# Optimization experiments

Measured on AMD Instinct MI355X. Metric: run time of the kernel, lower is better.

## Reference

```python
import jax, jax.numpy as jnp
import numpy as np

B, T, C, HS = 4, 512, 128, 64

def setup_inputs() -> dict:
    key = jax.random.key(0)
    ks = jax.random.split(key, 8)
    s1 = 1.0 / np.sqrt(2 * C)  # torch Linear default init scale ~ U(-1/sqrt(in),1/sqrt(in))
    s2 = 1.0 / np.sqrt(C)
    return {
        "x": jax.random.normal(ks[0], (B, T, C), jnp.float32),
        "pos_emb": jax.random.normal(ks[1], (T, C), jnp.float32),
        # att2 layer 1: Linear(2C -> C); stored as [2C, C] (in, out)
        "W1": jax.random.uniform(ks[2], (2 * C, C), jnp.float32, -s1, s1),
        "b1": jax.random.uniform(ks[3], (C,), jnp.float32, -s1, s1),
        # att2 layer 2: Linear(C -> 1)
        "W2": jax.random.uniform(ks[4], (C, 1), jnp.float32, -s2, s2),
        "b2": jax.random.uniform(ks[5], (1,), jnp.float32, -s2, s2),
        # value: Linear(C -> HS, bias=False)
        "Wv": jax.random.uniform(ks[6], (C, HS), jnp.float32, -s2, s2),
    }


def reference(x, pos_emb, W1, b1, W2, b2, Wv):
    b, t, c = x.shape
    x1 = pos_emb + x  # [b,t,c]
    # Pairwise feature: cat([x1[j], x1[i]], -1) at position [i, j].
    # First Linear on the concat splits into two [c,c] blocks -> avoids
    # materializing the [b,t,t,2c] concat while computing identical math.
    W1k, W1q = W1[:c], W1[c:]            # rows for k-part (x1[j]) and q-part (x1[i])
    Ak = jnp.einsum('bjc,cd->bjd', x1, W1k)  # [b,t,c] contribution from key index j
    Aq = jnp.einsum('bic,cd->bid', x1, W1q)  # [b,t,c] contribution from query index i
    hidden = jax.nn.relu(Aq[:, :, None, :] + Ak[:, None, :, :] + b1)  # [b,t,t,c]
    wei = (jnp.einsum('bijc,co->bijo', hidden, W2)[..., 0] + b2[0]) * (c ** -0.5)  # [b,t,t]
    # causal mask (tril)
    mask = jnp.tril(jnp.ones((t, t), dtype=bool))
    wei = jnp.where(mask, wei, -jnp.inf)
    wei = jax.nn.softmax(wei, axis=-1)
    v = jnp.einsum('btc,ch->bth', x, Wv)  # [b,t,hs]
    out = jnp.einsum('bij,bjh->bih', wei, v)
    return out
```

## Files before the change

kernel.cpp:

```cpp
#include <hip/hip_runtime.h>
#include <math.h>

#define B_ 4
#define T_ 512
#define C_ 128
#define HS_ 64

typedef float f4 __attribute__((ext_vector_type(4)));

#define SCALE_ 0.08838834764831845f

__global__ __launch_bounds__(640) void k_prep(
    const float* __restrict__ x, const float* __restrict__ pos,
    const float* __restrict__ W1, const float* __restrict__ b1,
    const float* __restrict__ Wv,
    float* __restrict__ Aq, float* __restrict__ AkT, float* __restrict__ V)
{
    __shared__ float x1s[8 * 132];
    __shared__ float xs[8 * 132];
    const int t = threadIdx.x;
    const int row0 = blockIdx.x * 8;

    if (t < 256) {
        int r = t >> 5, cq = t & 31;
        int gr = row0 + r;
        f4 xv = *(const f4*)(x + gr * 128 + cq * 4);
        f4 pv = *(const f4*)(pos + (gr & 511) * 128 + cq * 4);
        *(f4*)&xs[r * 132 + cq * 4] = xv;
        *(f4*)&x1s[r * 132 + cq * 4] = xv + pv;
    }
    __syncthreads();

    const int q = t >> 3;
    const int r = t & 7;

    const float* wbase;
    int wstr, col0;
    const float* xb;
    f4 binit = {0.f, 0.f, 0.f, 0.f};
    if (q < 32) {
        col0 = q * 4;
        wbase = W1 + 128 * 128 + col0;
        wstr = 128;
        xb = x1s;
        binit = *(const f4*)(b1 + col0);
    } else if (q < 64) {
        col0 = (q - 32) * 4;
        wbase = W1 + col0;
        wstr = 128;
        xb = x1s;
    } else {
        col0 = (q - 64) * 4;
        wbase = Wv + col0;
        wstr = 64;
        xb = xs;
    }

    f4 acc = binit;
    const float* xr = xb + r * 132;
#pragma unroll 8
    for (int c = 0; c < 128; ++c) {
        f4 w = *(const f4*)(wbase + c * wstr);
        acc += xr[c] * w;
    }

    const int gr = row0 + r;
    if (q < 32) {
        *(f4*)(Aq + (size_t)gr * 128 + col0) = acc;
    } else if (q < 64) {
        const int bb = gr >> 9, j = gr & 511;
        float* base = AkT + ((size_t)bb * 128 + col0) * 512 + j;
        base[0]    = acc.x;
        base[512]  = acc.y;
        base[1024] = acc.z;
        base[1536] = acc.w;
    } else {
        *(f4*)(V + (size_t)gr * 64 + col0) = acc;
    }
}

__global__ __launch_bounds__(256) void k_fusedp(
    const float* __restrict__ Aq, const float* __restrict__ AkT,
    const float* __restrict__ V, const float* __restrict__ W2,
    float* __restrict__ pml, float* __restrict__ pacc)
{
    __shared__ float aks[128][64];
    __shared__ float aqs[16][128];
    __shared__ float w2s[128];
    __shared__ float pbuf[4][4][64];

    const int t = threadIdx.x;
    const int b = blockIdx.y;
    const int f = blockIdx.x;

    int n = (int)((1.0f + sqrtf(1.0f + 2.0f * (float)f)) * 0.5f);
    while (2 * n * (n - 1) > f) --n;
    while (2 * n * (n + 1) <= f) ++n;
    const int rem = f - 2 * n * (n - 1);
    const int G = 4 * (n - 1) + rem / n;
    const int w = rem % n;
    const int j0 = w * 64;
    const int row0 = G * 16;

    const float* aktw = AkT + (size_t)b * 128 * 512 + j0;
    for (int idx = t; idx < 2048; idx += 256) {
        int c = idx >> 4, qq = idx & 15;
        *(f4*)&aks[c][qq * 4] = *(const f4*)(aktw + (size_t)c * 512 + qq * 4);
    }
    const float* aqg = Aq + (size_t)(b * 512 + row0) * 128;
    for (int idx = t; idx < 512; idx += 256) {
        int r = idx >> 5, cq = idx & 31;
        *(f4*)&aqs[r][cq * 4] = *(const f4*)(aqg + r * 128 + cq * 4);
    }
    if (t < 32) *(f4*)&w2s[t * 4] = *(const f4*)(W2 + t * 4);
    __syncthreads();

    const int w8 = t >> 6;
    const int lane = t & 63;
    const int rb = 4 * w8;
    const int r0 = row0 + rb, r1 = r0 + 1, r2 = r0 + 2, r3 = r0 + 3;
    const int gj = j0 + lane;

    float m0 = -1e30f, m1 = -1e30f, m2 = -1e30f, m3 = -1e30f;
    float l0 = 0.f, l1 = 0.f, l2 = 0.f, l3 = 0.f;
    float a0 = 0.f, a1 = 0.f, a2 = 0.f, a3 = 0.f;

    if (r3 >= j0) {
        float s0 = 0.f, s1 = 0.f, s2 = 0.f, s3 = 0.f;
#pragma unroll 4
        for (int c = 0; c < 128; ++c) {
            const float ak = aks[c][lane];
            const float wv = w2s[c];
            s0 += fmaxf(ak + aqs[rb + 0][c], 0.f) * wv;
            s1 += fmaxf(ak + aqs[rb + 1][c], 0.f) * wv;
            s2 += fmaxf(ak + aqs[rb + 2][c], 0.f) * wv;
            s3 += fmaxf(ak + aqs[rb + 3][c], 0.f) * wv;
        }
        s0 = (gj <= r0) ? s0 * SCALE_ : -1e30f;
        s1 = (gj <= r1) ? s1 * SCALE_ : -1e30f;
        s2 = (gj <= r2) ? s2 * SCALE_ : -1e30f;
        s3 = (gj <= r3) ? s3 * SCALE_ : -1e30f;

        float t0 = s0, t1 = s1, t2 = s2, t3 = s3;
#pragma unroll
        for (int off = 1; off < 64; off <<= 1) {
            t0 = fmaxf(t0, __shfl_xor(t0, off));
            t1 = fmaxf(t1, __shfl_xor(t1, off));
            t2 = fmaxf(t2, __shfl_xor(t2, off));
            t3 = fmaxf(t3, __shfl_xor(t3, off));
        }
        const float p0 = __expf(s0 - t0);
        const float p1 = __expf(s1 - t1);
        const float p2 = __expf(s2 - t2);
        const float p3 = __expf(s3 - t3);
        pbuf[w8][0][lane] = p0;
        pbuf[w8][1][lane] = p1;
        pbuf[w8][2][lane] = p2;
        pbuf[w8][3][lane] = p3;
        float u0 = p0, u1 = p1, u2 = p2, u3 = p3;
#pragma unroll
        for (int off = 1; off < 64; off <<= 1) {
            u0 += __shfl_xor(u0, off);
            u1 += __shfl_xor(u1, off);
            u2 += __shfl_xor(u2, off);
            u3 += __shfl_xor(u3, off);
        }

        const float* vt = V + ((size_t)b * 512 + j0) * 64 + lane;
        float b0 = 0.f, b1v = 0.f, b2v = 0.f, b3 = 0.f;
#pragma unroll 4
        for (int q4 = 0; q4 < 16; ++q4) {
            f4 q0 = *(const f4*)&pbuf[w8][0][q4 * 4];
            f4 q1 = *(const f4*)&pbuf[w8][1][q4 * 4];
            f4 q2 = *(const f4*)&pbuf[w8][2][q4 * 4];
            f4 q3 = *(const f4*)&pbuf[w8][3][q4 * 4];
            const float v0 = vt[(q4 * 4 + 0) * 64];
            const float v1 = vt[(q4 * 4 + 1) * 64];
            const float v2 = vt[(q4 * 4 + 2) * 64];
            const float v3 = vt[(q4 * 4 + 3) * 64];
            b0  += q0.x * v0 + q0.y * v1 + q0.z * v2 + q0.w * v3;
            b1v += q1.x * v0 + q1.y * v1 + q1.z * v2 + q1.w * v3;
            b2v += q2.x * v0 + q2.y * v1 + q2.z * v2 + q2.w * v3;
            b3  += q3.x * v0 + q3.y * v1 + q3.z * v2 + q3.w * v3;
        }

        const bool c0 = (r0 >= j0), c1 = (r1 >= j0), c2 = (r2 >= j0);
        m0 = c0 ? t0 : -1e30f;  l0 = c0 ? u0 : 0.f;  a0 = c0 ? b0 : 0.f;
        m1 = c1 ? t1 : -1e30f;  l1 = c1 ? u1 : 0.f;  a1 = c1 ? b1v : 0.f;
        m2 = c2 ? t2 : -1e30f;  l2 = c2 ? u2 : 0.f;  a2 = c2 ? b2v : 0.f;
        m3 = t3;                l3 = u3;             a3 = b3;
    }

    const size_t k0 = ((size_t)(b * 512 + r0) * 8 + w);
    pacc[(k0 + 0 ) * 64 + lane] = a0;
    pacc[(k0 + 8 ) * 64 + lane] = a1;
    pacc[(k0 + 16) * 64 + lane] = a2;
    pacc[(k0 + 24) * 64 + lane] = a3;
    if (lane == 0) {
        pml[(k0 + 0 ) * 2] = m0;  pml[(k0 + 0 ) * 2 + 1] = l0;
        pml[(k0 + 8 ) * 2] = m1;  pml[(k0 + 8 ) * 2 + 1] = l1;
        pml[(k0 + 16) * 2] = m2;  pml[(k0 + 16) * 2 + 1] = l2;
        pml[(k0 + 24) * 2] = m3;  pml[(k0 + 24) * 2 + 1] = l3;
    }
}

__global__ __launch_bounds__(256) void k_merge(
    const float* __restrict__ pml, const float* __restrict__ pacc,
    float* __restrict__ out)
{
    const int t = threadIdx.x;
    const int w8 = t >> 6, lane = t & 63;
    const int grow = blockIdx.x * 4 + w8;
    const int i = grow & 511;
    const int nw = (i >> 6) + 1;
    const size_t base = (size_t)grow * 8;

    float ms = -1e30f;
    for (int w = 0; w < nw; ++w) ms = fmaxf(ms, pml[(base + w) * 2]);
    float num = 0.f, den = 0.f;
    for (int w = 0; w < nw; ++w) {
        const float e = __expf(pml[(base + w) * 2] - ms);
        den += pml[(base + w) * 2 + 1] * e;
        num += pacc[(base + w) * 64 + lane] * e;
    }
    out[(size_t)grow * 64 + lane] = num / den;
}

extern "C" void kernel_launch(void* const* d_in, const int* in_sizes, int n_in,
                              void* d_out, int out_size, void* d_ws, size_t ws_size,
                              hipStream_t stream)
{
    const float* x   = (const float*)d_in[0];
    const float* pos = (const float*)d_in[1];
    const float* W1  = (const float*)d_in[2];
    const float* b1  = (const float*)d_in[3];
    const float* W2  = (const float*)d_in[4];
    const float* b2  = (const float*)d_in[5];  (void)b2;
    const float* Wv  = (const float*)d_in[6];
    float* out = (float*)d_out;
    float* ws = (float*)d_ws;

    float* Aq   = ws;
    float* AkT  = ws + 262144;
    float* V    = ws + 524288;
    float* pml  = ws + 655360;
    float* pacc = ws + 688128;

    k_prep<<<dim3(256), dim3(640), 0, stream>>>(x, pos, W1, b1, Wv, Aq, AkT, V);
    k_fusedp<<<dim3(144, B_), dim3(256), 0, stream>>>(Aq, AkT, V, W2, pml, pacc);
    k_merge<<<dim3(512), dim3(256), 0, stream>>>(pml, pacc, out);
}
```

Baseline: 39.49 us.

## Store Ak row-major with XOR-swizzled LDS and vectorize the pairwise MLP loop

Ak is now written row-major by the prep kernel instead of being scattered into a transposed layout. The fused kernel stages it into shared memory with an XOR swizzle so that each lane can read its own key row as float4 without bank conflicts. The hidden-layer reduction is rewritten to process four channels per iteration with vector adds and FMAs, which cuts LDS load instruction count. The cost is a different summation order and extra register pressure from the four f4 accumulators.

```diff
diff --git a/kernel.cpp b/kernel.cpp
--- a/kernel.cpp
+++ b/kernel.cpp
@@ -14,7 +14,7 @@
     const float* __restrict__ x, const float* __restrict__ pos,
     const float* __restrict__ W1, const float* __restrict__ b1,
     const float* __restrict__ Wv,
-    float* __restrict__ Aq, float* __restrict__ AkT, float* __restrict__ V)
+    float* __restrict__ Aq, float* __restrict__ Ak, float* __restrict__ V)
 {
     __shared__ float x1s[8 * 132];
     __shared__ float xs[8 * 132];
@@ -37,23 +37,31 @@
     const float* wbase;
     int wstr, col0;
     const float* xb;
+    float* obase;
+    int ostr;
     f4 binit = {0.f, 0.f, 0.f, 0.f};
     if (q < 32) {
         col0 = q * 4;
         wbase = W1 + 128 * 128 + col0;
         wstr = 128;
         xb = x1s;
+        obase = Aq;
+        ostr = 128;
         binit = *(const f4*)(b1 + col0);
     } else if (q < 64) {
         col0 = (q - 32) * 4;
         wbase = W1 + col0;
         wstr = 128;
         xb = x1s;
+        obase = Ak;
+        ostr = 128;
     } else {
         col0 = (q - 64) * 4;
         wbase = Wv + col0;
         wstr = 64;
         xb = xs;
+        obase = V;
+        ostr = 64;
     }
 
     f4 acc = binit;
@@ -65,26 +73,15 @@
     }
 
     const int gr = row0 + r;
-    if (q < 32) {
-        *(f4*)(Aq + (size_t)gr * 128 + col0) = acc;
-    } else if (q < 64) {
-        const int bb = gr >> 9, j = gr & 511;
-        float* base = AkT + ((size_t)bb * 128 + col0) * 512 + j;
-        base[0]    = acc.x;
-        base[512]  = acc.y;
-        base[1024] = acc.z;
-        base[1536] = acc.w;
-    } else {
-        *(f4*)(V + (size_t)gr * 64 + col0) = acc;
-    }
+    *(f4*)(obase + (size_t)gr * ostr + col0) = acc;
 }
 
 __global__ __launch_bounds__(256) void k_fusedp(
-    const float* __restrict__ Aq, const float* __restrict__ AkT,
+    const float* __restrict__ Aq, const float* __restrict__ Ak,
     const float* __restrict__ V, const float* __restrict__ W2,
     float* __restrict__ pml, float* __restrict__ pacc)
 {
-    __shared__ float aks[128][64];
+    __shared__ float aks[64 * 128];
     __shared__ float aqs[16][128];
     __shared__ float w2s[128];
     __shared__ float pbuf[4][4][64];
@@ -102,10 +99,11 @@
     const int j0 = w * 64;
     const int row0 = G * 16;
 
-    const float* aktw = AkT + (size_t)b * 128 * 512 + j0;
+    const float* akg = Ak + ((size_t)b * 512 + j0) * 128;
     for (int idx = t; idx < 2048; idx += 256) {
-        int c = idx >> 4, qq = idx & 15;
-        *(f4*)&aks[c][qq * 4] = *(const f4*)(aktw + (size_t)c * 512 + qq * 4);
+        int r = idx >> 5, cq = idx & 31;
+        *(f4*)&aks[r * 128 + ((cq ^ (r & 7)) << 2)] =
+            *(const f4*)(akg + r * 128 + cq * 4);
     }
     const float* aqg = Aq + (size_t)(b * 512 + row0) * 128;
     for (int idx = t; idx < 512; idx += 256) {
@@ -126,16 +124,35 @@
     float a0 = 0.f, a1 = 0.f, a2 = 0.f, a3 = 0.f;
 
     if (r3 >= j0) {
-        float s0 = 0.f, s1 = 0.f, s2 = 0.f, s3 = 0.f;
-#pragma unroll 4
-        for (int c = 0; c < 128; ++c) {
-            const float ak = aks[c][lane];
-            const float wv = w2s[c];
-            s0 += fmaxf(ak + aqs[rb + 0][c], 0.f) * wv;
-            s1 += fmaxf(ak + aqs[rb + 1][c], 0.f) * wv;
-            s2 += fmaxf(ak + aqs[rb + 2][c], 0.f) * wv;
-            s3 += fmaxf(ak + aqs[rb + 3][c], 0.f) * wv;
-        }
+        const float* akrow = &aks[lane * 128];
+        const int swz = lane & 7;
+        f4 v0 = {0.f, 0.f, 0.f, 0.f}, v1 = v0, v2 = v0, v3 = v0;
+#pragma unroll 8
+        for (int cq = 0; cq < 32; ++cq) {
+            const int c = cq * 4;
+            const f4 akv = *(const f4*)(akrow + ((cq ^ swz) << 2));
+            const f4 wv  = *(const f4*)&w2s[c];
+            f4 t0v = akv + *(const f4*)&aqs[rb + 0][c];
+            f4 t1v = akv + *(const f4*)&aqs[rb + 1][c];
+            f4 t2v = akv + *(const f4*)&aqs[rb + 2][c];
+            f4 t3v = akv + *(const f4*)&aqs[rb + 3][c];
+            t0v.x = fmaxf(t0v.x, 0.f); t0v.y = fmaxf(t0v.y, 0.f);
+            t0v.z = fmaxf(t0v.z, 0.f); t0v.w = fmaxf(t0v.w, 0.f);
+            t1v.x = fmaxf(t1v.x, 0.f); t1v.y = fmaxf(t1v.y, 0.f);
+            t1v.z = fmaxf(t1v.z, 0.f); t1v.w = fmaxf(t1v.w, 0.f);
+            t2v.x = fmaxf(t2v.x, 0.f); t2v.y = fmaxf(t2v.y, 0.f);
+            t2v.z = fmaxf(t2v.z, 0.f); t2v.w = fmaxf(t2v.w, 0.f);
+            t3v.x = fmaxf(t3v.x, 0.f); t3v.y = fmaxf(t3v.y, 0.f);
+            t3v.z = fmaxf(t3v.z, 0.f); t3v.w = fmaxf(t3v.w, 0.f);
+            v0 += t0v * wv;
+            v1 += t1v * wv;
+            v2 += t2v * wv;
+            v3 += t3v * wv;
+        }
+        float s0 = (v0.x + v0.y) + (v0.z + v0.w);
+        float s1 = (v1.x + v1.y) + (v1.z + v1.w);
+        float s2 = (v2.x + v2.y) + (v2.z + v2.w);
+        float s3 = (v3.x + v3.y) + (v3.z + v3.w);
         s0 = (gj <= r0) ? s0 * SCALE_ : -1e30f;
         s1 = (gj <= r1) ? s1 * SCALE_ : -1e30f;
         s2 = (gj <= r2) ? s2 * SCALE_ : -1e30f;
@@ -174,14 +191,14 @@
             f4 q1 = *(const f4*)&pbuf[w8][1][q4 * 4];
             f4 q2 = *(const f4*)&pbuf[w8][2][q4 * 4];
             f4 q3 = *(const f4*)&pbuf[w8][3][q4 * 4];
-            const float v0 = vt[(q4 * 4 + 0) * 64];
-            const float v1 = vt[(q4 * 4 + 1) * 64];
-            const float v2 = vt[(q4 * 4 + 2) * 64];
-            const float v3 = vt[(q4 * 4 + 3) * 64];
-            b0  += q0.x * v0 + q0.y * v1 + q0.z * v2 + q0.w * v3;
-            b1v += q1.x * v0 + q1.y * v1 + q1.z * v2 + q1.w * v3;
-            b2v += q2.x * v0 + q2.y * v1 + q2.z * v2 + q2.w * v3;
-            b3  += q3.x * v0 + q3.y * v1 + q3.z * v2 + q3.w * v3;
+            const float vv0 = vt[(q4 * 4 + 0) * 64];
+            const float vv1 = vt[(q4 * 4 + 1) * 64];
+            const float vv2 = vt[(q4 * 4 + 2) * 64];
+            const float vv3 = vt[(q4 * 4 + 3) * 64];
+            b0  += q0.x * vv0 + q0.y * vv1 + q0.z * vv2 + q0.w * vv3;
+            b1v += q1.x * vv0 + q1.y * vv1 + q1.z * vv2 + q1.w * vv3;
+            b2v += q2.x * vv0 + q2.y * vv1 + q2.z * vv2 + q2.w * vv3;
+            b3  += q3.x * vv0 + q3.y * vv1 + q3.z * vv2 + q3.w * vv3;
         }
 
         const bool c0 = (r0 >= j0), c1 = (r1 >= j0), c2 = (r2 >= j0);
@@ -241,12 +258,12 @@
     float* ws = (float*)d_ws;
 
     float* Aq   = ws;
-    float* AkT  = ws + 262144;
+    float* Ak   = ws + 262144;
     float* V    = ws + 524288;
     float* pml  = ws + 655360;
     float* pacc = ws + 688128;
 
-    k_prep<<<dim3(256), dim3(640), 0, stream>>>(x, pos, W1, b1, Wv, Aq, AkT, V);
-    k_fusedp<<<dim3(144, B_), dim3(256), 0, stream>>>(Aq, AkT, V, W2, pml, pacc);
+    k_prep<<<dim3(256), dim3(640), 0, stream>>>(x, pos, W1, b1, Wv, Aq, Ak, V);
+    k_fusedp<<<dim3(144, B_), dim3(256), 0, stream>>>(Aq, Ak, V, W2, pml, pacc);
     k_merge<<<dim3(512), dim3(256), 0, stream>>>(pml, pacc, out);
 }
```

Measured after the change: 40.67 us. +3.0%, slower.

## Drop shared-memory staging in pairwise score kernel, read Aq/AkT directly from global

Applied to the files above, without the earlier changes.

The fused score kernel no longer stages the AkT tile, Aq rows and W2 in LDS behind a block barrier. Each wave now reads its Aq rows and W2 as wave-uniform vector loads and AkT columns per lane straight from global memory. The softmax finalisation is restructured per row, with live-row masking replacing the previous whole-warp skip branch. This removes LDS fill time and the syncthreads, but relies on cache hits for repeated global reads and makes fully masked waves still compute.

```diff
diff --git a/kernel.cpp b/kernel.cpp
--- a/kernel.cpp
+++ b/kernel.cpp
@@ -81,12 +81,9 @@
 
 __global__ __launch_bounds__(256) void k_fusedp(
     const float* __restrict__ Aq, const float* __restrict__ AkT,
-    const float* __restrict__ V, const float* __restrict__ W2,
+    const float* __restrict__ Vv, const float* __restrict__ W2,
     float* __restrict__ pml, float* __restrict__ pacc)
 {
-    __shared__ float aks[128][64];
-    __shared__ float aqs[16][128];
-    __shared__ float w2s[128];
     __shared__ float pbuf[4][4][64];
 
     const int t = threadIdx.x;
@@ -100,95 +97,76 @@
     const int G = 4 * (n - 1) + rem / n;
     const int w = rem % n;
     const int j0 = w * 64;
-    const int row0 = G * 16;
-
-    const float* aktw = AkT + (size_t)b * 128 * 512 + j0;
-    for (int idx = t; idx < 2048; idx += 256) {
-        int c = idx >> 4, qq = idx & 15;
-        *(f4*)&aks[c][qq * 4] = *(const f4*)(aktw + (size_t)c * 512 + qq * 4);
-    }
-    const float* aqg = Aq + (size_t)(b * 512 + row0) * 128;
-    for (int idx = t; idx < 512; idx += 256) {
-        int r = idx >> 5, cq = idx & 31;
-        *(f4*)&aqs[r][cq * 4] = *(const f4*)(aqg + r * 128 + cq * 4);
-    }
-    if (t < 32) *(f4*)&w2s[t * 4] = *(const f4*)(W2 + t * 4);
-    __syncthreads();
-
-    const int w8 = t >> 6;
-    const int lane = t & 63;
-    const int rb = 4 * w8;
-    const int r0 = row0 + rb, r1 = r0 + 1, r2 = r0 + 2, r3 = r0 + 3;
+
+    const int w8 = t >> 6, lane = t & 63;
+    const int r0 = G * 16 + w8 * 4;
     const int gj = j0 + lane;
 
-    float m0 = -1e30f, m1 = -1e30f, m2 = -1e30f, m3 = -1e30f;
-    float l0 = 0.f, l1 = 0.f, l2 = 0.f, l3 = 0.f;
+    const float* aq0 = Aq + (size_t)(b * 512 + r0) * 128;
+    const float* aq1 = aq0 + 128;
+    const float* aq2 = aq1 + 128;
+    const float* aq3 = aq2 + 128;
+    const float* akc = AkT + (size_t)b * 65536 + gj;
+
+    float s0 = 0.f, s1 = 0.f, s2 = 0.f, s3 = 0.f;
+#pragma unroll 8
+    for (int cq = 0; cq < 32; ++cq) {
+        const f4 q0 = *(const f4*)(aq0 + cq * 4);
+        const f4 q1 = *(const f4*)(aq1 + cq * 4);
+        const f4 q2 = *(const f4*)(aq2 + cq * 4);
+        const f4 q3 = *(const f4*)(aq3 + cq * 4);
+        const f4 wq = *(const f4*)(W2 + cq * 4);
+#pragma unroll
+        for (int ch = 0; ch < 4; ++ch) {
+            const float ak = akc[(size_t)(cq * 4 + ch) * 512];
+            s0 += fmaxf(ak + q0[ch], 0.f) * wq[ch];
+            s1 += fmaxf(ak + q1[ch], 0.f) * wq[ch];
+            s2 += fmaxf(ak + q2[ch], 0.f) * wq[ch];
+            s3 += fmaxf(ak + q3[ch], 0.f) * wq[ch];
+        }
+    }
+
+    float m0, m1, m2, m3, l0, l1, l2, l3;
+#define FINROW(R, SS, MD, LD)                                            \
+    {                                                                    \
+        const int rr_ = r0 + (R);                                        \
+        float sx = (gj <= rr_) ? (SS) * SCALE_ : -1e30f;                 \
+        float mx = sx;                                                   \
+        _Pragma("unroll")                                                \
+        for (int off = 1; off < 64; off <<= 1)                           \
+            mx = fmaxf(mx, __shfl_xor(mx, off));                         \
+        const bool live_ = (j0 <= rr_);                                  \
+        const float p = live_ ? __expf(sx - mx) : 0.f;                   \
+        pbuf[w8][R][lane] = p;                                           \
+        float ls = p;                                                    \
+        _Pragma("unroll")                                                \
+        for (int off = 1; off < 64; off <<= 1)                           \
+            ls += __shfl_xor(ls, off);                                   \
+        MD = live_ ? mx : -1e30f;                                        \
+        LD = ls;                                                         \
+    }
+    FINROW(0, s0, m0, l0)
+    FINROW(1, s1, m1, l1)
+    FINROW(2, s2, m2, l2)
+    FINROW(3, s3, m3, l3)
+#undef FINROW
+
+    const float* vt = Vv + ((size_t)b * 512 + j0) * 64 + lane;
     float a0 = 0.f, a1 = 0.f, a2 = 0.f, a3 = 0.f;
-
-    if (r3 >= j0) {
-        float s0 = 0.f, s1 = 0.f, s2 = 0.f, s3 = 0.f;
 #pragma unroll 4
-        for (int c = 0; c < 128; ++c) {
-            const float ak = aks[c][lane];
-            const float wv = w2s[c];
-            s0 += fmaxf(ak + aqs[rb + 0][c], 0.f) * wv;
-            s1 += fmaxf(ak + aqs[rb + 1][c], 0.f) * wv;
-            s2 += fmaxf(ak + aqs[rb + 2][c], 0.f) * wv;
-            s3 += fmaxf(ak + aqs[rb + 3][c], 0.f) * wv;
-        }
-        s0 = (gj <= r0) ? s0 * SCALE_ : -1e30f;
-        s1 = (gj <= r1) ? s1 * SCALE_ : -1e30f;
-        s2 = (gj <= r2) ? s2 * SCALE_ : -1e30f;
-        s3 = (gj <= r3) ? s3 * SCALE_ : -1e30f;
-
-        float t0 = s0, t1 = s1, t2 = s2, t3 = s3;
-#pragma unroll
-        for (int off = 1; off < 64; off <<= 1) {
-            t0 = fmaxf(t0, __shfl_xor(t0, off));
-            t1 = fmaxf(t1, __shfl_xor(t1, off));
-            t2 = fmaxf(t2, __shfl_xor(t2, off));
-            t3 = fmaxf(t3, __shfl_xor(t3, off));
-        }
-        const float p0 = __expf(s0 - t0);
-        const float p1 = __expf(s1 - t1);
-        const float p2 = __expf(s2 - t2);
-        const float p3 = __expf(s3 - t3);
-        pbuf[w8][0][lane] = p0;
-        pbuf[w8][1][lane] = p1;
-        pbuf[w8][2][lane] = p2;
-        pbuf[w8][3][lane] = p3;
-        float u0 = p0, u1 = p1, u2 = p2, u3 = p3;
-#pragma unroll
-        for (int off = 1; off < 64; off <<= 1) {
-            u0 += __shfl_xor(u0, off);
-            u1 += __shfl_xor(u1, off);
-            u2 += __shfl_xor(u2, off);
-            u3 += __shfl_xor(u3, off);
-        }
-
-        const float* vt = V + ((size_t)b * 512 + j0) * 64 + lane;
-        float b0 = 0.f, b1v = 0.f, b2v = 0.f, b3 = 0.f;
-#pragma unroll 4
-        for (int q4 = 0; q4 < 16; ++q4) {
-            f4 q0 = *(const f4*)&pbuf[w8][0][q4 * 4];
-            f4 q1 = *(const f4*)&pbuf[w8][1][q4 * 4];
-            f4 q2 = *(const f4*)&pbuf[w8][2][q4 * 4];
-            f4 q3 = *(const f4*)&pbuf[w8][3][q4 * 4];
-            const float v0 = vt[(q4 * 4 + 0) * 64];
-            const float v1 = vt[(q4 * 4 + 1) * 64];
-            const float v2 = vt[(q4 * 4 + 2) * 64];
-            const float v3 = vt[(q4 * 4 + 3) * 64];
-            b0  += q0.x * v0 + q0.y * v1 + q0.z * v2 + q0.w * v3;
-            b1v += q1.x * v0 + q1.y * v1 + q1.z * v2 + q1.w * v3;
-            b2v += q2.x * v0 + q2.y * v1 + q2.z * v2 + q2.w * v3;
-            b3  += q3.x * v0 + q3.y * v1 + q3.z * v2 + q3.w * v3;
-        }
-
-        const bool c0 = (r0 >= j0), c1 = (r1 >= j0), c2 = (r2 >= j0);
-        m0 = c0 ? t0 : -1e30f;  l0 = c0 ? u0 : 0.f;  a0 = c0 ? b0 : 0.f;
-        m1 = c1 ? t1 : -1e30f;  l1 = c1 ? u1 : 0.f;  a1 = c1 ? b1v : 0.f;
-        m2 = c2 ? t2 : -1e30f;  l2 = c2 ? u2 : 0.f;  a2 = c2 ? b2v : 0.f;
-        m3 = t3;                l3 = u3;             a3 = b3;
+    for (int q4 = 0; q4 < 16; ++q4) {
+        const f4 p0 = *(const f4*)&pbuf[w8][0][q4 * 4];
+        const f4 p1 = *(const f4*)&pbuf[w8][1][q4 * 4];
+        const f4 p2 = *(const f4*)&pbuf[w8][2][q4 * 4];
+        const f4 p3 = *(const f4*)&pbuf[w8][3][q4 * 4];
+        const float v0 = vt[(q4 * 4 + 0) * 64];
+        const float v1 = vt[(q4 * 4 + 1) * 64];
+        const float v2 = vt[(q4 * 4 + 2) * 64];
+        const float v3 = vt[(q4 * 4 + 3) * 64];
+        a0 += p0.x * v0 + p0.y * v1 + p0.z * v2 + p0.w * v3;
+        a1 += p1.x * v0 + p1.y * v1 + p1.z * v2 + p1.w * v3;
+        a2 += p2.x * v0 + p2.y * v1 + p2.z * v2 + p2.w * v3;
+        a3 += p3.x * v0 + p3.y * v1 + p3.z * v2 + p3.w * v3;
     }
 
     const size_t k0 = ((size_t)(b * 512 + r0) * 8 + w);
```

Result: slower. 66.49 us (+68.4%).
